# Kernel optimization log

Hardware: AMD Instinct MI355X
Metric: run time of the kernel (lower is better)

## Reference

```python
import jax, jax.numpy as jnp
import numpy as np
import math

S, B, F, H = 2048, 4, 512, 8
D = F // H  # head_dim = 64
THETA = 10000.0


def setup_inputs() -> dict:
    key = jax.random.key(0)
    ks = jax.random.split(key, 11)
    mk = lambda k, shape, scale=1.0: (jax.random.normal(k, shape, dtype=jnp.float32) * scale)
    s = 1.0 / math.sqrt(F)
    return {
        "q": mk(ks[0], (S, B, F)),
        "k": mk(ks[1], (S, B, F)),
        "v": mk(ks[2], (S, B, F)),
        "Wq": mk(ks[3], (F, F), s), "bq": mk(ks[4], (F,), s),
        "Wk": mk(ks[5], (F, F), s), "bk": mk(ks[6], (F,), s),
        "Wv": mk(ks[7], (F, F), s), "bv": mk(ks[8], (F,), s),
        "Wo": mk(ks[9], (F, F), s), "bo": mk(ks[10], (F,), s),
    }


def _to_batches(x):
    # (S, B, F) -> (B*H, S, D)
    return x.reshape(S, B, H, D).transpose(1, 2, 0, 3).reshape(B * H, S, D)


def _from_batches(y):
    # (B*H, S, D) -> (S, B, F)
    return y.reshape(B, H, S, D).transpose(2, 0, 1, 3).reshape(S, B, F)


def _rope(x):
    # interleaved RoPE on (B*H, S, D): pairs (even, odd) are (real, imag)
    xr = x.reshape(B * H, S, D // 2, 2)
    real, imag = xr[..., 0], xr[..., 1]
    thetas = THETA ** (-2.0 * jnp.arange(D // 2, dtype=jnp.float32) / D)  # (D/2,)
    ang = jnp.arange(S, dtype=jnp.float32)[:, None] * thetas[None, :]     # (S, D/2)
    cos, sin = jnp.cos(ang), jnp.sin(ang)
    even = real * cos - imag * sin
    odd = real * sin + imag * cos
    return jnp.stack([even, odd], axis=-1).reshape(B * H, S, D)


def reference(q, k, v, Wq, bq, Wk, bk, Wv, bv, Wo, bo):
    relu = jax.nn.relu
    q = relu(jnp.einsum('sbf,gf->sbg', q, Wq) + bq)
    k = relu(jnp.einsum('sbf,gf->sbg', k, Wk) + bk)
    v = relu(jnp.einsum('sbf,gf->sbg', v, Wv) + bv)
    q, k, v = _to_batches(q), _to_batches(k), _to_batches(v)
    q, k = _rope(q), _rope(k)
    scores = jnp.einsum('nqd,nkd->nqk', q, k) / math.sqrt(D)  # (B*H, S, S)
    attn = jax.nn.softmax(scores, axis=-1)
    y = jnp.einsum('nqk,nkd->nqd', attn, v)
    y = _from_batches(y)
    return relu(jnp.einsum('sbf,gf->sbg', y, Wo) + bo)
```

## Files before the change

### kernel.cpp

```cpp
#include <hip/hip_runtime.h>
#include <math.h>

#define S_LEN 2048
#define BATCH 4
#define FDIM 512
#define NHEAD 8
#define DHEAD 64

typedef unsigned short u16;
typedef short bf16x8 __attribute__((ext_vector_type(8)));
typedef float f32x4 __attribute__((ext_vector_type(4)));

__device__ __forceinline__ u16 f2bf(float f) {
    unsigned u = __float_as_uint(f);
    return (u16)((u + 0x7fffu + ((u >> 16) & 1u)) >> 16);
}
__device__ __forceinline__ float bf2f(u16 u) {
    return __uint_as_float(((unsigned)u) << 16);
}
__device__ __forceinline__ ushort4 f2bf4(float4 t) {
    return (ushort4){f2bf(t.x), f2bf(t.y), f2bf(t.z), f2bf(t.w)};
}

__global__ __launch_bounds__(256) void gemm_qkv(
    const float* __restrict__ Aq, const float* __restrict__ Ak, const float* __restrict__ Av,
    const float* __restrict__ Wq, const float* __restrict__ Wk, const float* __restrict__ Wv,
    const float* __restrict__ bq, const float* __restrict__ bk, const float* __restrict__ bv,
    u16* __restrict__ Qb, u16* __restrict__ Kb, u16* __restrict__ Vtb, float qscale)
{
    __shared__ __align__(16) u16 pool[24576];
    const int tid = threadIdx.x;
    const int w = tid >> 6, lane = tid & 63;
    const int quad = lane >> 4, l16 = lane & 15;
    const int m0 = blockIdx.x * 128, n0 = blockIdx.y * 64, z = blockIdx.z;

    const float* A = (z == 0) ? Aq : (z == 1) ? Ak : Av;
    const float* W = (z == 0) ? Wq : (z == 1) ? Wk : Wv;
    const float* bias = (z == 0) ? bq : (z == 1) ? bk : bv;
    const float qs = (z == 0) ? qscale : 1.0f;

    const int srow = tid >> 4, scol = (tid & 15) * 4;

    f32x4 acc[2][4];
    #pragma unroll
    for (int rt = 0; rt < 2; rt++)
        #pragma unroll
        for (int nt = 0; nt < 4; nt++) acc[rt][nt] = (f32x4){0.f, 0.f, 0.f, 0.f};

    ushort4 ap[8], bp[4];
    auto loadT = [&](int k0) {
        #pragma unroll
        for (int it = 0; it < 8; it++) {
            int r = srow + it * 16;
            ap[it] = f2bf4(*(const float4*)(A + (size_t)(m0 + r) * FDIM + k0 + scol));
        }
        #pragma unroll
        for (int it = 0; it < 4; it++) {
            int r = srow + it * 16;
            bp[it] = f2bf4(*(const float4*)(W + (size_t)(n0 + r) * FDIM + k0 + scol));
        }
    };
    auto storeT = [&](int buf) {
        u16* Ab = pool + buf * 8192;
        u16* Bb = pool + 16384 + buf * 4096;
        #pragma unroll
        for (int it = 0; it < 8; it++) {
            int r = srow + it * 16;
            *(ushort4*)(Ab + r * 64 + (((scol >> 3) ^ (r & 7)) * 8) + (scol & 7)) = ap[it];
        }
        #pragma unroll
        for (int it = 0; it < 4; it++) {
            int r = srow + it * 16;
            *(ushort4*)(Bb + r * 64 + (((scol >> 3) ^ (r & 7)) * 8) + (scol & 7)) = bp[it];
        }
    };
    auto compute = [&](int buf) {
        const u16* Ab = pool + buf * 8192;
        const u16* Bb = pool + 16384 + buf * 4096;
        bf16x8 af[2][2];
        #pragma unroll
        for (int rt = 0; rt < 2; rt++) {
            const int row = w * 32 + rt * 16 + l16;
            af[rt][0] = *(const bf16x8*)(Ab + row * 64 + (((0 + quad) ^ (l16 & 7)) * 8));
            af[rt][1] = *(const bf16x8*)(Ab + row * 64 + (((4 + quad) ^ (l16 & 7)) * 8));
        }
        #pragma unroll
        for (int nt = 0; nt < 4; nt++) {
            const int rowb = nt * 16 + l16;
            bf16x8 b0 = *(const bf16x8*)(Bb + rowb * 64 + (((0 + quad) ^ (l16 & 7)) * 8));
            bf16x8 b1 = *(const bf16x8*)(Bb + rowb * 64 + (((4 + quad) ^ (l16 & 7)) * 8));
            #pragma unroll
            for (int rt = 0; rt < 2; rt++) {
                acc[rt][nt] = __builtin_amdgcn_mfma_f32_16x16x32_bf16(af[rt][0], b0, acc[rt][nt], 0, 0, 0);
                acc[rt][nt] = __builtin_amdgcn_mfma_f32_16x16x32_bf16(af[rt][1], b1, acc[rt][nt], 0, 0, 0);
            }
        }
    };

    loadT(0); storeT(0); __syncthreads();
    int cur = 0;
    #pragma unroll
    for (int i = 0; i < 8; i++) {
        if (i < 7) loadT((i + 1) * 64);
        compute(cur);
        if (i < 7) { storeT(1 - cur); cur = 1 - cur; __syncthreads(); }
    }

    float bvv[4];
    #pragma unroll
    for (int nt = 0; nt < 4; nt++) bvv[nt] = bias[n0 + nt * 16 + l16];
    const int h = blockIdx.y;
    u16* Epi = pool;

    if (z < 2) {
        u16* outB = (z == 0) ? Qb : Kb;
        const float NEG_LN1E4_32 = -0.2878231366242558f;
        float th[4];
        #pragma unroll
        for (int nt = 0; nt < 4; nt++)
            th[nt] = expf(NEG_LN1E4_32 * (float)(nt * 8 + (l16 >> 1)));
        #pragma unroll
        for (int pass = 0; pass < 2; pass++) {
            #pragma unroll
            for (int rt = 0; rt < 2; rt++) {
                const int s = (m0 >> 2) + w * 8 + rt * 4 + quad;
                #pragma unroll
                for (int nn = 0; nn < 2; nn++) {
                    const int nt = pass * 2 + nn;
                    float c, sn;
                    __sincosf((float)s * th[nt], &sn, &c);
                    #pragma unroll
                    for (int i = 0; i < 4; i++) {
                        float vv = fmaxf(acc[rt][nt][i] + bvv[nt], 0.f);
                        float t = __shfl_xor(vv, 1);
                        vv = (l16 & 1) ? (t * sn + vv * c) : (vv * c - t * sn);
                        Epi[(w * 32 + rt * 16 + quad * 4 + i) * 40 + nn * 16 + l16] = f2bf(vv * qs);
                    }
                }
            }
            asm volatile("s_waitcnt lgkmcnt(0)" ::: "memory");
            const int mloc = lane >> 1, seg = lane & 1;
            const int m = m0 + w * 32 + mloc;
            const int s2 = m >> 2, b = m & 3;
            const size_t dst = ((size_t)(b * 8 + h) * S_LEN + s2) * DHEAD + pass * 32 + seg * 16;
            uint4 t0 = *(const uint4*)&Epi[(w * 32 + mloc) * 40 + seg * 16];
            uint4 t1 = *(const uint4*)&Epi[(w * 32 + mloc) * 40 + seg * 16 + 8];
            *(uint4*)(outB + dst)     = t0;
            *(uint4*)(outB + dst + 8) = t1;
            asm volatile("s_waitcnt lgkmcnt(0)" ::: "memory");
        }
    } else {
        #pragma unroll
        for (int pass = 0; pass < 2; pass++) {
            #pragma unroll
            for (int rt = 0; rt < 2; rt++)
                #pragma unroll
                for (int nn = 0; nn < 2; nn++) {
                    const int nt = pass * 2 + nn;
                    #pragma unroll
                    for (int i = 0; i < 4; i++) {
                        float vv = fmaxf(acc[rt][nt][i] + bvv[nt], 0.f);
                        Epi[(w * 32 + rt * 16 + quad * 4 + i) * 40 + nn * 16 + l16] = f2bf(vv);
                    }
                }
            asm volatile("s_waitcnt lgkmcnt(0)" ::: "memory");
            const int half = lane >> 5, dp = lane & 31;
            const int d = pass * 32 + dp;
            const int sBase = (m0 >> 2) + w * 8;
            #pragma unroll
            for (int bb = 0; bb < 2; bb++) {
                const int b = half * 2 + bb;
                u16 tmp[8];
                #pragma unroll
                for (int sl = 0; sl < 8; sl++)
                    tmp[sl] = Epi[(w * 32 + sl * 4 + b) * 40 + dp];
                *(uint4*)(Vtb + ((size_t)(b * 8 + h) * DHEAD + d) * S_LEN + sBase) =
                    *(const uint4*)tmp;
            }
            asm volatile("s_waitcnt lgkmcnt(0)" ::: "memory");
        }
    }
}

__global__ __launch_bounds__(256) void gemm_out(
    const u16* __restrict__ A, const float* __restrict__ W,
    const float* __restrict__ bias, float* __restrict__ outF)
{
    __shared__ __align__(16) u16 pool[24576];
    const int tid = threadIdx.x;
    const int w = tid >> 6, lane = tid & 63;
    const int quad = lane >> 4, l16 = lane & 15;
    const int m0 = blockIdx.x * 128, n0 = blockIdx.y * 64;

    const int srow = tid >> 4, scol = (tid & 15) * 4;
    int rr[4], gg[4];
    #pragma unroll
    for (int it = 0; it < 4; it++) { int c = tid + it * 256; rr[it] = c >> 3; gg[it] = c & 7; }

    f32x4 acc[2][4];
    #pragma unroll
    for (int rt = 0; rt < 2; rt++)
        #pragma unroll
        for (int nt = 0; nt < 4; nt++) acc[rt][nt] = (f32x4){0.f, 0.f, 0.f, 0.f};

    uint4 av[4]; ushort4 bp[4];
    auto loadT = [&](int k0) {
        #pragma unroll
        for (int it = 0; it < 4; it++)
            av[it] = *(const uint4*)(A + (size_t)(m0 + rr[it]) * FDIM + k0 + gg[it] * 8);
        #pragma unroll
        for (int it = 0; it < 4; it++) {
            int r = srow + it * 16;
            bp[it] = f2bf4(*(const float4*)(W + (size_t)(n0 + r) * FDIM + k0 + scol));
        }
    };
    auto storeT = [&](int buf) {
        u16* Ab = pool + buf * 8192;
        u16* Bb = pool + 16384 + buf * 4096;
        #pragma unroll
        for (int it = 0; it < 4; it++)
            *(uint4*)(Ab + rr[it] * 64 + ((gg[it] ^ (rr[it] & 7)) * 8)) = av[it];
        #pragma unroll
        for (int it = 0; it < 4; it++) {
            int r = srow + it * 16;
            *(ushort4*)(Bb + r * 64 + (((scol >> 3) ^ (r & 7)) * 8) + (scol & 7)) = bp[it];
        }
    };
    auto compute = [&](int buf) {
        const u16* Ab = pool + buf * 8192;
        const u16* Bb = pool + 16384 + buf * 4096;
        bf16x8 af[2][2];
        #pragma unroll
        for (int rt = 0; rt < 2; rt++) {
            const int row = w * 32 + rt * 16 + l16;
            af[rt][0] = *(const bf16x8*)(Ab + row * 64 + (((0 + quad) ^ (l16 & 7)) * 8));
            af[rt][1] = *(const bf16x8*)(Ab + row * 64 + (((4 + quad) ^ (l16 & 7)) * 8));
        }
        #pragma unroll
        for (int nt = 0; nt < 4; nt++) {
            const int rowb = nt * 16 + l16;
            bf16x8 b0 = *(const bf16x8*)(Bb + rowb * 64 + (((0 + quad) ^ (l16 & 7)) * 8));
            bf16x8 b1 = *(const bf16x8*)(Bb + rowb * 64 + (((4 + quad) ^ (l16 & 7)) * 8));
            #pragma unroll
            for (int rt = 0; rt < 2; rt++) {
                acc[rt][nt] = __builtin_amdgcn_mfma_f32_16x16x32_bf16(af[rt][0], b0, acc[rt][nt], 0, 0, 0);
                acc[rt][nt] = __builtin_amdgcn_mfma_f32_16x16x32_bf16(af[rt][1], b1, acc[rt][nt], 0, 0, 0);
            }
        }
    };

    loadT(0); storeT(0); __syncthreads();
    int cur = 0;
    #pragma unroll
    for (int i = 0; i < 8; i++) {
        if (i < 7) loadT((i + 1) * 64);
        compute(cur);
        if (i < 7) { storeT(1 - cur); cur = 1 - cur; __syncthreads(); }
    }

    float bvv[4];
    #pragma unroll
    for (int nt = 0; nt < 4; nt++) bvv[nt] = bias[n0 + nt * 16 + l16];
    #pragma unroll
    for (int rt = 0; rt < 2; rt++)
        #pragma unroll
        for (int nt = 0; nt < 4; nt++)
            #pragma unroll
            for (int i = 0; i < 4; i++) {
                const int m = m0 + w * 32 + rt * 16 + quad * 4 + i;
                outF[(size_t)m * FDIM + n0 + nt * 16 + l16] =
                    fmaxf(acc[rt][nt][i] + bvv[nt], 0.f);
            }
}

__global__ __launch_bounds__(256, 4) void flash_attn_mfma(
    const u16* __restrict__ Q, const u16* __restrict__ K, const u16* __restrict__ Vt,
    u16* __restrict__ Opart, float* __restrict__ Lpart)
{
    __shared__ __align__(16) u16 pool[16384];
    const int tid = threadIdx.x;
    const int w = tid >> 6, lane = tid & 63;
    const int quad = lane >> 4, l16 = lane & 15;
    const int s0 = blockIdx.x * 128, n = blockIdx.y, kh = blockIdx.z;

    const size_t baseQ = ((size_t)n * S_LEN + s0) * DHEAD;
    const size_t baseK = ((size_t)n * S_LEN + kh * 1024) * DHEAD;
    const size_t baseV = (size_t)n * DHEAD * S_LEN + kh * 1024;

    #pragma unroll
    for (int it = 0; it < 4; it++) {
        int c = tid + it * 256, r = c >> 3, g = c & 7;
        *(uint4*)(pool + r * 64 + ((g ^ (r & 7)) * 8)) =
            *(const uint4*)(Q + baseQ + r * DHEAD + g * 8);
    }
    __syncthreads();
    const int xa = ((0 + quad) ^ (l16 & 7)) * 8;
    const int xb = ((4 + quad) ^ (l16 & 7)) * 8;
    bf16x8 qa[2][2];
    #pragma unroll
    for (int s = 0; s < 2; s++) {
        const int row = w * 32 + s * 16 + l16;
        qa[s][0] = *(const bf16x8*)(pool + row * 64 + xa);
        qa[s][1] = *(const bf16x8*)(pool + row * 64 + xb);
    }
    __syncthreads();

    f32x4 accO[2][4];
    #pragma unroll
    for (int s = 0; s < 2; s++)
        #pragma unroll
        for (int dt = 0; dt < 4; dt++) accO[s][dt] = (f32x4){0.f, 0.f, 0.f, 0.f};
    float lsum[2] = {0.f, 0.f};

    const int sr = tid >> 3, sg = tid & 7;
    const int Hh = sg >> 2, vOff = ((sg >> 1) & 1) * 4;
    const int o1 = (2 * sg) & 3, o2 = (2 * sg + 1) & 3;
    uint4 kc[2], vc[2];
    auto loadKV = [&](int k0) {
        kc[0] = *(const uint4*)(K + baseK + (size_t)(k0 + sr) * DHEAD + sg * 8);
        kc[1] = *(const uint4*)(K + baseK + (size_t)(k0 + sr + 32) * DHEAD + sg * 8);
        vc[0] = *(const uint4*)(Vt + baseV + (size_t)sr * S_LEN + k0 + sg * 8);
        vc[1] = *(const uint4*)(Vt + baseV + (size_t)(sr + 32) * S_LEN + k0 + sg * 8);
    };
    auto storeKV = [&](int buf) {
        u16* Kb = pool + buf * 8192;
        u16* Vb = pool + 4096 + buf * 8192;
        const int swk = (sg ^ (sr & 7)) * 8;
        *(uint4*)(Kb + sr * 64 + swk)        = kc[0];
        *(uint4*)(Kb + (sr + 32) * 64 + swk) = kc[1];
        const int a1 = ((Hh * 4 + o1) ^ (sr & 7)) * 8 + vOff;
        const int a2 = ((Hh * 4 + o2) ^ (sr & 7)) * 8 + vOff;
        *(uint2*)(Vb + sr * 64 + a1)        = (uint2){vc[0].x, vc[0].y};
        *(uint2*)(Vb + sr * 64 + a2)        = (uint2){vc[0].z, vc[0].w};
        *(uint2*)(Vb + (sr + 32) * 64 + a1) = (uint2){vc[1].x, vc[1].y};
        *(uint2*)(Vb + (sr + 32) * 64 + a2) = (uint2){vc[1].z, vc[1].w};
    };

    loadKV(0);
    storeKV(0);
    __syncthreads();

    for (int i = 0; i < 16; i++) {
        const int buf = i & 1;
        const u16* Kbf = pool + buf * 8192;
        const u16* Vbf = pool + 4096 + buf * 8192;
        if (i < 15) loadKV((i + 1) * 64);

        f32x4 sc[2][4];
        #pragma unroll
        for (int kt = 0; kt < 4; kt++) {
            const int kr = kt * 16 + l16;
            bf16x8 kb0 = *(const bf16x8*)(Kbf + kr * 64 + xa);
            bf16x8 kb1 = *(const bf16x8*)(Kbf + kr * 64 + xb);
            #pragma unroll
            for (int s = 0; s < 2; s++) {
                f32x4 z = (f32x4){0.f, 0.f, 0.f, 0.f};
                z = __builtin_amdgcn_mfma_f32_16x16x32_bf16(kb0, qa[s][0], z, 0, 0, 0);
                z = __builtin_amdgcn_mfma_f32_16x16x32_bf16(kb1, qa[s][1], z, 0, 0, 0);
                sc[s][kt] = z;
            }
        }

        union { unsigned u[4]; bf16x8 v; } pb[2][2];
        #pragma unroll
        for (int s = 0; s < 2; s++) {
            unsigned dw[8];
            #pragma unroll
            for (int kt = 0; kt < 4; kt++) {
                float p0 = __builtin_amdgcn_exp2f(sc[s][kt][0] - 20.0f);
                float p1 = __builtin_amdgcn_exp2f(sc[s][kt][1] - 20.0f);
                float p2 = __builtin_amdgcn_exp2f(sc[s][kt][2] - 20.0f);
                float p3 = __builtin_amdgcn_exp2f(sc[s][kt][3] - 20.0f);
                dw[kt * 2 + 0] = __builtin_amdgcn_perm(__float_as_uint(p1), __float_as_uint(p0), 0x07060302u);
                dw[kt * 2 + 1] = __builtin_amdgcn_perm(__float_as_uint(p3), __float_as_uint(p2), 0x07060302u);
            }
            float a = 0.f;
            #pragma unroll
            for (int t = 0; t < 8; t++) {
                a += __uint_as_float(dw[t] << 16);
                a += __uint_as_float(dw[t] & 0xFFFF0000u);
            }
            lsum[s] += a;
            #pragma unroll
            for (int t = 0; t < 4; t++) { pb[s][0].u[t] = dw[t]; pb[s][1].u[t] = dw[4 + t]; }
        }

        #pragma unroll
        for (int dt = 0; dt < 4; dt++) {
            const int vr = dt * 16 + l16;
            bf16x8 va0 = *(const bf16x8*)(Vbf + vr * 64 + xa);
            bf16x8 va1 = *(const bf16x8*)(Vbf + vr * 64 + xb);
            #pragma unroll
            for (int s = 0; s < 2; s++) {
                accO[s][dt] = __builtin_amdgcn_mfma_f32_16x16x32_bf16(va0, pb[s][0].v, accO[s][dt], 0, 0, 0);
                accO[s][dt] = __builtin_amdgcn_mfma_f32_16x16x32_bf16(va1, pb[s][1].v, accO[s][dt], 0, 0, 0);
            }
        }

        if (i < 15) { storeKV(1 - buf); __syncthreads(); }
    }

    const int bI = n >> 3, h = n & 7;
    u16* Ob = Opart + (size_t)kh * (8192 * 512);
    #pragma unroll
    for (int s = 0; s < 2; s++) {
        float l = lsum[s];
        l += __shfl_xor(l, 16);
        l += __shfl_xor(l, 32);
        const int qg = s0 + w * 32 + s * 16 + l16;
        if (quad == 0)
            Lpart[(size_t)kh * 65536 + n * 2048 + qg] = l;
        const size_t base = (size_t)(qg * BATCH + bI) * FDIM + h * DHEAD;
        #pragma unroll
        for (int dt = 0; dt < 4; dt++) {
            ushort4 st = {f2bf(accO[s][dt][0]), f2bf(accO[s][dt][1]),
                          f2bf(accO[s][dt][2]), f2bf(accO[s][dt][3])};
            *(ushort4*)(Ob + base + dt * 16 + quad * 4) = st;
        }
    }
}

__global__ __launch_bounds__(256) void combine_k(
    const u16* __restrict__ O, const float* __restrict__ L, u16* __restrict__ Yb)
{
    const int idx = blockIdx.x * 256 + threadIdx.x;
    const int m = idx >> 7, c4 = idx & 127;
    const int g = c4 * 4, h = g >> 6;
    const int q = m >> 2, b = m & 3, n = b * 8 + h;
    const float l = L[n * 2048 + q] + L[65536 + n * 2048 + q];
    const float inv = 1.0f / l;
    const ushort4 o0 = *(const ushort4*)(O + (size_t)m * 512 + g);
    const ushort4 o1 = *(const ushort4*)(O + 4194304u + (size_t)m * 512 + g);
    ushort4 r = {f2bf((bf2f(o0.x) + bf2f(o1.x)) * inv),
                 f2bf((bf2f(o0.y) + bf2f(o1.y)) * inv),
                 f2bf((bf2f(o0.z) + bf2f(o1.z)) * inv),
                 f2bf((bf2f(o0.w) + bf2f(o1.w)) * inv)};
    *(ushort4*)(Yb + (size_t)m * 512 + g) = r;
}

extern "C" void kernel_launch(void* const* d_in, const int* in_sizes, int n_in,
                              void* d_out, int out_size, void* d_ws, size_t ws_size,
                              hipStream_t stream) {
    const float* q  = (const float*)d_in[0];
    const float* k  = (const float*)d_in[1];
    const float* v  = (const float*)d_in[2];
    const float* Wq = (const float*)d_in[3];
    const float* bq = (const float*)d_in[4];
    const float* Wk = (const float*)d_in[5];
    const float* bk = (const float*)d_in[6];
    const float* Wv = (const float*)d_in[7];
    const float* bv = (const float*)d_in[8];
    const float* Wo = (const float*)d_in[9];
    const float* bo = (const float*)d_in[10];
    float* out = (float*)d_out;

    const int NIN = S_LEN * BATCH * FDIM;
    u16* p = (u16*)d_ws;
    u16* Qb  = p;             p += NIN;
    u16* Kb  = p;             p += NIN;
    u16* Vtb = p;             p += NIN;
    u16* Opart = p;           p += 2 * NIN;
    float* Lpart = (float*)p;
    u16* Yb = Qb;

    const float QSCALE = 0.125f * 1.4426950408889634f;

    dim3 blk(256);
    dim3 gQKV(S_LEN * BATCH / 128, FDIM / 64, 3);
    gemm_qkv<<<gQKV, blk, 0, stream>>>(q, k, v, Wq, Wk, Wv, bq, bk, bv,
                                       Qb, Kb, Vtb, QSCALE);

    dim3 gAttn(S_LEN / 128, 32, 2);
    flash_attn_mfma<<<gAttn, blk, 0, stream>>>(Qb, Kb, Vtb, Opart, Lpart);

    combine_k<<<4096, blk, 0, stream>>>(Opart, Lpart, Yb);

    dim3 gOut(S_LEN * BATCH / 128, FDIM / 64);
    gemm_out<<<gOut, blk, 0, stream>>>(Yb, Wo, bo, out);
}
```

Baseline: 221.3 us.

## Compute softmax row sums with MFMA ones-vector and shrink output GEMM tile

```diff
diff --git a/kernel.cpp b/kernel.cpp
--- a/kernel.cpp
+++ b/kernel.cpp
@@ -186,27 +186,25 @@
     const u16* __restrict__ A, const float* __restrict__ W,
     const float* __restrict__ bias, float* __restrict__ outF)
 {
-    __shared__ __align__(16) u16 pool[24576];
+    __shared__ __align__(16) u16 pool[16384];
     const int tid = threadIdx.x;
     const int w = tid >> 6, lane = tid & 63;
     const int quad = lane >> 4, l16 = lane & 15;
-    const int m0 = blockIdx.x * 128, n0 = blockIdx.y * 64;
+    const int m0 = blockIdx.x * 64, n0 = blockIdx.y * 64;
 
     const int srow = tid >> 4, scol = (tid & 15) * 4;
-    int rr[4], gg[4];
-    #pragma unroll
-    for (int it = 0; it < 4; it++) { int c = tid + it * 256; rr[it] = c >> 3; gg[it] = c & 7; }
-
-    f32x4 acc[2][4];
-    #pragma unroll
-    for (int rt = 0; rt < 2; rt++)
-        #pragma unroll
-        for (int nt = 0; nt < 4; nt++) acc[rt][nt] = (f32x4){0.f, 0.f, 0.f, 0.f};
-
-    uint4 av[4]; ushort4 bp[4];
+    int rr[2], gg[2];
+    #pragma unroll
+    for (int it = 0; it < 2; it++) { int c = tid + it * 256; rr[it] = c >> 3; gg[it] = c & 7; }
+
+    f32x4 acc[4];
+    #pragma unroll
+    for (int nt = 0; nt < 4; nt++) acc[nt] = (f32x4){0.f, 0.f, 0.f, 0.f};
+
+    uint4 av[2]; ushort4 bp[4];
     auto loadT = [&](int k0) {
         #pragma unroll
-        for (int it = 0; it < 4; it++)
+        for (int it = 0; it < 2; it++)
             av[it] = *(const uint4*)(A + (size_t)(m0 + rr[it]) * FDIM + k0 + gg[it] * 8);
         #pragma unroll
         for (int it = 0; it < 4; it++) {
@@ -215,10 +213,10 @@
         }
     };
     auto storeT = [&](int buf) {
-        u16* Ab = pool + buf * 8192;
-        u16* Bb = pool + 16384 + buf * 4096;
-        #pragma unroll
-        for (int it = 0; it < 4; it++)
+        u16* Ab = pool + buf * 4096;
+        u16* Bb = pool + 8192 + buf * 4096;
+        #pragma unroll
+        for (int it = 0; it < 2; it++)
             *(uint4*)(Ab + rr[it] * 64 + ((gg[it] ^ (rr[it] & 7)) * 8)) = av[it];
         #pragma unroll
         for (int it = 0; it < 4; it++) {
@@ -227,25 +225,18 @@
         }
     };
     auto compute = [&](int buf) {
-        const u16* Ab = pool + buf * 8192;
-        const u16* Bb = pool + 16384 + buf * 4096;
-        bf16x8 af[2][2];
-        #pragma unroll
-        for (int rt = 0; rt < 2; rt++) {
-            const int row = w * 32 + rt * 16 + l16;
-            af[rt][0] = *(const bf16x8*)(Ab + row * 64 + (((0 + quad) ^ (l16 & 7)) * 8));
-            af[rt][1] = *(const bf16x8*)(Ab + row * 64 + (((4 + quad) ^ (l16 & 7)) * 8));
-        }
+        const u16* Ab = pool + buf * 4096;
+        const u16* Bb = pool + 8192 + buf * 4096;
+        const int row = w * 16 + l16;
+        bf16x8 af0 = *(const bf16x8*)(Ab + row * 64 + (((0 + quad) ^ (l16 & 7)) * 8));
+        bf16x8 af1 = *(const bf16x8*)(Ab + row * 64 + (((4 + quad) ^ (l16 & 7)) * 8));
         #pragma unroll
         for (int nt = 0; nt < 4; nt++) {
             const int rowb = nt * 16 + l16;
             bf16x8 b0 = *(const bf16x8*)(Bb + rowb * 64 + (((0 + quad) ^ (l16 & 7)) * 8));
             bf16x8 b1 = *(const bf16x8*)(Bb + rowb * 64 + (((4 + quad) ^ (l16 & 7)) * 8));
-            #pragma unroll
-            for (int rt = 0; rt < 2; rt++) {
-                acc[rt][nt] = __builtin_amdgcn_mfma_f32_16x16x32_bf16(af[rt][0], b0, acc[rt][nt], 0, 0, 0);
-                acc[rt][nt] = __builtin_amdgcn_mfma_f32_16x16x32_bf16(af[rt][1], b1, acc[rt][nt], 0, 0, 0);
-            }
+            acc[nt] = __builtin_amdgcn_mfma_f32_16x16x32_bf16(af0, b0, acc[nt], 0, 0, 0);
+            acc[nt] = __builtin_amdgcn_mfma_f32_16x16x32_bf16(af1, b1, acc[nt], 0, 0, 0);
         }
     };
 
@@ -262,15 +253,13 @@
     #pragma unroll
     for (int nt = 0; nt < 4; nt++) bvv[nt] = bias[n0 + nt * 16 + l16];
     #pragma unroll
-    for (int rt = 0; rt < 2; rt++)
-        #pragma unroll
-        for (int nt = 0; nt < 4; nt++)
-            #pragma unroll
-            for (int i = 0; i < 4; i++) {
-                const int m = m0 + w * 32 + rt * 16 + quad * 4 + i;
-                outF[(size_t)m * FDIM + n0 + nt * 16 + l16] =
-                    fmaxf(acc[rt][nt][i] + bvv[nt], 0.f);
-            }
+    for (int nt = 0; nt < 4; nt++)
+        #pragma unroll
+        for (int i = 0; i < 4; i++) {
+            const int m = m0 + w * 16 + quad * 4 + i;
+            outF[(size_t)m * FDIM + n0 + nt * 16 + l16] =
+                fmaxf(acc[nt][i] + bvv[nt], 0.f);
+        }
 }
 
 __global__ __launch_bounds__(256, 4) void flash_attn_mfma(
@@ -305,12 +294,17 @@
     }
     __syncthreads();
 
-    f32x4 accO[2][4];
-    #pragma unroll
-    for (int s = 0; s < 2; s++)
+    union { unsigned u[4]; bf16x8 v; } onesA;
+    #pragma unroll
+    for (int t = 0; t < 4; t++) onesA.u[t] = 0x3F803F80u;
+
+    f32x4 accO[2][4], accL[2];
+    #pragma unroll
+    for (int s = 0; s < 2; s++) {
         #pragma unroll
         for (int dt = 0; dt < 4; dt++) accO[s][dt] = (f32x4){0.f, 0.f, 0.f, 0.f};
-    float lsum[2] = {0.f, 0.f};
+        accL[s] = (f32x4){0.f, 0.f, 0.f, 0.f};
+    }
 
     const int sr = tid >> 3, sg = tid & 7;
     const int Hh = sg >> 2, vOff = ((sg >> 1) & 1) * 4;
@@ -364,25 +358,23 @@
         union { unsigned u[4]; bf16x8 v; } pb[2][2];
         #pragma unroll
         for (int s = 0; s < 2; s++) {
-            unsigned dw[8];
             #pragma unroll
             for (int kt = 0; kt < 4; kt++) {
                 float p0 = __builtin_amdgcn_exp2f(sc[s][kt][0] - 20.0f);
                 float p1 = __builtin_amdgcn_exp2f(sc[s][kt][1] - 20.0f);
                 float p2 = __builtin_amdgcn_exp2f(sc[s][kt][2] - 20.0f);
                 float p3 = __builtin_amdgcn_exp2f(sc[s][kt][3] - 20.0f);
-                dw[kt * 2 + 0] = __builtin_amdgcn_perm(__float_as_uint(p1), __float_as_uint(p0), 0x07060302u);
-                dw[kt * 2 + 1] = __builtin_amdgcn_perm(__float_as_uint(p3), __float_as_uint(p2), 0x07060302u);
-            }
-            float a = 0.f;
-            #pragma unroll
-            for (int t = 0; t < 8; t++) {
-                a += __uint_as_float(dw[t] << 16);
-                a += __uint_as_float(dw[t] & 0xFFFF0000u);
-            }
-            lsum[s] += a;
-            #pragma unroll
-            for (int t = 0; t < 4; t++) { pb[s][0].u[t] = dw[t]; pb[s][1].u[t] = dw[4 + t]; }
+                pb[s][kt >> 1].u[(kt & 1) * 2 + 0] =
+                    __builtin_amdgcn_perm(__float_as_uint(p1), __float_as_uint(p0), 0x07060302u);
+                pb[s][kt >> 1].u[(kt & 1) * 2 + 1] =
+                    __builtin_amdgcn_perm(__float_as_uint(p3), __float_as_uint(p2), 0x07060302u);
+            }
+        }
+
+        #pragma unroll
+        for (int s = 0; s < 2; s++) {
+            accL[s] = __builtin_amdgcn_mfma_f32_16x16x32_bf16(onesA.v, pb[s][0].v, accL[s], 0, 0, 0);
+            accL[s] = __builtin_amdgcn_mfma_f32_16x16x32_bf16(onesA.v, pb[s][1].v, accL[s], 0, 0, 0);
         }
 
         #pragma unroll
@@ -404,12 +396,9 @@
     u16* Ob = Opart + (size_t)kh * (8192 * 512);
     #pragma unroll
     for (int s = 0; s < 2; s++) {
-        float l = lsum[s];
-        l += __shfl_xor(l, 16);
-        l += __shfl_xor(l, 32);
         const int qg = s0 + w * 32 + s * 16 + l16;
         if (quad == 0)
-            Lpart[(size_t)kh * 65536 + n * 2048 + qg] = l;
+            Lpart[(size_t)kh * 65536 + n * 2048 + qg] = accL[s][0];
         const size_t base = (size_t)(qg * BATCH + bI) * FDIM + h * DHEAD;
         #pragma unroll
         for (int dt = 0; dt < 4; dt++) {
@@ -475,6 +464,6 @@
 
     combine_k<<<4096, blk, 0, stream>>>(Opart, Lpart, Yb);
 
-    dim3 gOut(S_LEN * BATCH / 128, FDIM / 64);
+    dim3 gOut(S_LEN * BATCH / 64, FDIM / 64);
     gemm_out<<<gOut, blk, 0, stream>>>(Yb, Wo, bo, out);
 }
```

After: 225.8 us. 1.02x slower.
